# Kernel optimization log

Measured on AMD Instinct MI355X. Metric: run time of the kernel, lower is better.

## Reference

```python
import jax, jax.numpy as jnp
import numpy as np

H, W, A, C = 200, 704, 2, 256   # BEV grid, anchors, feature channels
NC, K = 4, 20000                # peer CAVs, selected anchors per CAV
REG = 7 * A                     # reg head channels


def setup_inputs() -> dict:
    key = jax.random.key(0)
    ks = jax.random.split(key, 8)
    feat = jax.random.normal(ks[0], (1, C, H, W), jnp.float32)
    cls_w = jax.random.normal(ks[1], (A, C), jnp.float32) * 0.02
    cls_b = jnp.zeros((A,), jnp.float32)
    reg_w = jax.random.normal(ks[2], (REG, C), jnp.float32) * 0.02
    reg_b = jnp.zeros((REG,), jnp.float32)
    psm_v2x = jax.random.normal(ks[3], (NC, K), jnp.float32)
    rm_v2x = jax.random.normal(ks[4], (NC, 7 * K), jnp.float32)
    scores_v2x = jax.random.uniform(ks[5], (NC, K), jnp.float32, 0.3, 1.0)
    flat = A * H * W
    idx = []
    for i in range(NC):  # unique sorted flat indices per CAV (masked_select semantics)
        perm = jax.random.permutation(jax.random.fold_in(ks[6], i), flat)[:K]
        idx.append(jnp.sort(perm))
    mask_idx = jnp.stack(idx).astype(jnp.int32)
    # mask_reg = mask.repeat(1,7,1,1): indices tile with offsets r*A*H*W
    offs = (jnp.arange(7) * flat).astype(jnp.int32)
    mask_reg_idx = (mask_idx[:, None, :] + offs[None, :, None]).reshape(NC, 7 * K)
    return {
        'spatial_features_2d': feat, 'cls_w': cls_w, 'cls_b': cls_b,
        'reg_w': reg_w, 'reg_b': reg_b, 'psm_v2x': psm_v2x, 'rm_v2x': rm_v2x,
        'scores_v2x': scores_v2x, 'mask_idx': mask_idx, 'mask_reg_idx': mask_reg_idx,
    }


def _restore(vals, idx, shape):
    # restore_tensor: scatter compacted values into zeros at flat indices, per CAV
    n = vals.shape[0]
    flat = int(np.prod(shape))
    out = jnp.zeros((n, flat), vals.dtype)
    out = out.at[jnp.arange(n)[:, None], idx].set(vals)
    return out.reshape((n,) + shape)


def reference(spatial_features_2d, cls_w, cls_b, reg_w, reg_b,
              psm_v2x, rm_v2x, scores_v2x, mask_idx, mask_reg_idx):
    # 1x1 conv heads
    psm_single = jnp.einsum('bchw,ac->bahw', spatial_features_2d, cls_w) + cls_b[None, :, None, None]
    rm_single = jnp.einsum('bchw,rc->brhw', spatial_features_2d, reg_w) + reg_b[None, :, None, None]
    prob = jax.nn.sigmoid(psm_single)
    # scatter-restore peer CAV results onto the BEV grid
    r_psm = _restore(psm_v2x, mask_idx, (A, H, W))        # [NC,A,H,W]
    r_scores = _restore(scores_v2x, mask_idx, (A, H, W))
    r_rm = _restore(rm_v2x, mask_reg_idx, (REG, H, W))    # [NC,14,H,W]
    psm_all = jnp.concatenate([psm_single, r_psm], axis=0)      # [1+NC,A,H,W]
    prob_all = jnp.concatenate([prob, r_scores], axis=0)
    rm_all = jnp.concatenate([rm_single, r_rm], axis=0)         # [1+NC,14,H,W]
    # per-cell winning CAV by score, then gather psm/rm from the winner
    cav = jnp.argmax(prob_all, axis=0)                    # [A,H,W]
    psm = jnp.take_along_axis(psm_all, cav[None], axis=0) # [1,A,H,W]
    cav_reg = jnp.tile(cav, (7, 1, 1))                    # [14,H,W]
    rm = jnp.take_along_axis(rm_all, cav_reg[None], axis=0)  # [1,14,H,W]
    return psm, rm
```

## Files before the change

### kernel.cpp

```cpp
#include <hip/hip_runtime.h>

#define HH 200
#define WW 704
#define HW (HH * WW)
#define HW2 (HW / 2)
#define AHW (2 * HW)
#define CC 256
#define NCAV 4
#define KK 20000
#define NJ 16
#define UPIPE 8

typedef unsigned int u32;

__global__ void scatter_best(const int* __restrict__ mask_idx,
                             const float* __restrict__ scores,
                             u32* __restrict__ winmap) {
    int t = blockIdx.x * blockDim.x + threadIdx.x;
    if (t >= NCAV * KK) return;
    int x = mask_idx[t];
    int n = t / KK;
    union { float f; u32 u; } s;
    s.f = scores[t];
    u32 pack = ((s.u - 0x3E800000u) << 7) | (u32)(3 - n);
    atomicMax(winmap + x, pack);
}

__device__ __forceinline__ int bsearch_row(const int* __restrict__ row, int x) {
    int lo = 0, hi = KK;
    while (lo < hi) {
        int mid = (lo + hi) >> 1;
        if (row[mid] < x) lo = mid + 1; else hi = mid;
    }
    return lo;
}

__global__ __launch_bounds__(64, 1) void head_select(
    const float2* __restrict__ feat2,
    const float* __restrict__ cls_w,
    const float* __restrict__ reg_w,
    const float* __restrict__ cls_b,
    const float* __restrict__ reg_b,
    const float* __restrict__ psm_v2x,
    const float* __restrict__ rm_v2x,
    const int* __restrict__ mask_idx,
    const u32* __restrict__ winmap,
    float* __restrict__ out) {
    __shared__ float w_lds[CC * NJ];

    int tid = threadIdx.x;
    for (int i = tid; i < CC * NJ; i += 64) {
        int j = i >> 8, c = i & 255;
        w_lds[c * NJ + j] = (j < 2) ? cls_w[j * CC + c] : reg_w[(j - 2) * CC + c];
    }
    __syncthreads();

    int q = blockIdx.x * 64 + tid;
    int pos = q * 2;

    float acc[2][NJ];
#pragma unroll
    for (int j = 0; j < NJ; ++j) {
        float b = (j < 2) ? cls_b[j] : reg_b[j - 2];
        acc[0][j] = b; acc[1][j] = b;
    }

    const float2* fp = feat2 + q;

    float2 A[UPIPE], B[UPIPE];
#pragma unroll
    for (int u = 0; u < UPIPE; ++u) A[u] = fp[u * HW2];

    for (int cb = 0; cb < CC; cb += 2 * UPIPE) {
#pragma unroll
        for (int u = 0; u < UPIPE; ++u) B[u] = fp[(cb + UPIPE + u) * HW2];
#pragma unroll
        for (int u = 0; u < UPIPE; ++u) {
            int c = cb + u;
            const float4* wv = (const float4*)&w_lds[c * NJ];
            float w[NJ];
            *(float4*)&w[0]  = wv[0];
            *(float4*)&w[4]  = wv[1];
            *(float4*)&w[8]  = wv[2];
            *(float4*)&w[12] = wv[3];
#pragma unroll
            for (int j = 0; j < NJ; ++j) {
                acc[0][j] += A[u].x * w[j];
                acc[1][j] += A[u].y * w[j];
            }
        }
#pragma unroll
        for (int u = 0; u < UPIPE; ++u) {
            int cn = cb + 2 * UPIPE + u;
            A[u] = fp[(cn < CC ? cn : 0) * HW2];
        }
#pragma unroll
        for (int u = 0; u < UPIPE; ++u) {
            int c = cb + UPIPE + u;
            const float4* wv = (const float4*)&w_lds[c * NJ];
            float w[NJ];
            *(float4*)&w[0]  = wv[0];
            *(float4*)&w[4]  = wv[1];
            *(float4*)&w[8]  = wv[2];
            *(float4*)&w[12] = wv[3];
#pragma unroll
            for (int j = 0; j < NJ; ++j) {
                acc[0][j] += B[u].x * w[j];
                acc[1][j] += B[u].y * w[j];
            }
        }
    }

    float2* out2 = (float2*)out;
#pragma unroll
    for (int a = 0; a < 2; ++a) {
        float ps[2], rm[7][2];
#pragma unroll
        for (int e = 0; e < 2; ++e) {
            float p = acc[e][a];
            float prob = 1.0f / (1.0f + expf(-p));
            int x = a * HW + pos + e;
            u32 win = winmap[x];
            float sc = 0.0f;
            if (win != 0u) {
                union { u32 u; float f; } v;
                v.u = (win >> 7) + 0x3E800000u;
                sc = v.f;
            }
            if (sc > prob) {
                int n = 3 - (int)(win & 3u);
                int k = bsearch_row(mask_idx + n * KK, x);
                ps[e] = psm_v2x[n * KK + k];
#pragma unroll
                for (int r = 0; r < 7; ++r)
                    rm[r][e] = rm_v2x[n * (7 * KK) + r * KK + k];
            } else {
                ps[e] = p;
#pragma unroll
                for (int r = 0; r < 7; ++r)
                    rm[r][e] = acc[e][2 + 2 * r + a];
            }
        }
        out2[a * HW2 + q] = make_float2(ps[0], ps[1]);
#pragma unroll
        for (int r = 0; r < 7; ++r)
            out2[HW + (2 * r + a) * HW2 + q] = make_float2(rm[r][0], rm[r][1]);
    }
}

extern "C" void kernel_launch(void* const* d_in, const int* in_sizes, int n_in,
                              void* d_out, int out_size, void* d_ws, size_t ws_size,
                              hipStream_t stream) {
    const float* feat    = (const float*)d_in[0];
    const float* cls_w   = (const float*)d_in[1];
    const float* cls_b   = (const float*)d_in[2];
    const float* reg_w   = (const float*)d_in[3];
    const float* reg_b   = (const float*)d_in[4];
    const float* psm_v2x = (const float*)d_in[5];
    const float* rm_v2x  = (const float*)d_in[6];
    const float* scores  = (const float*)d_in[7];
    const int* mask_idx  = (const int*)d_in[8];

    const size_t win_bytes = (size_t)AHW * sizeof(u32);
    u32* winmap = (ws_size >= win_bytes) ? (u32*)d_ws : (u32*)d_in[9];

    hipMemsetAsync(winmap, 0, win_bytes, stream);

    scatter_best<<<(NCAV * KK + 255) / 256, 256, 0, stream>>>(mask_idx, scores, winmap);
    head_select<<<HW2 / 64, 64, 0, stream>>>(
        (const float2*)feat, cls_w, reg_w, cls_b, reg_b,
        psm_v2x, rm_v2x, mask_idx, winmap, (float*)d_out);
}
```

Before: 249.4 us.

## Split channel reduction across four waves per block with LDS reduction

Each block now uses four wavefronts, and each wave accumulates a 64-channel slice of the 1x1 conv for the same 128 pixels. The partial sums go to LDS and are reduced by the first 128 threads, which then run the sigmoid, the winner selection and the output writes. This gives more waves per CU and more loads in flight to hide memory latency in a bandwidth-bound kernel. In exchange it adds two block barriers and an LDS reduction, leaves only half the threads active in the epilogue, and replaces float2 output stores with scalar stores.

```diff
diff --git a/kernel.cpp b/kernel.cpp
--- a/kernel.cpp
+++ b/kernel.cpp
@@ -10,6 +10,7 @@
 #define KK 20000
 #define NJ 16
 #define UPIPE 8
+#define CPW 64
 
 typedef unsigned int u32;
 
@@ -35,7 +36,7 @@
     return lo;
 }
 
-__global__ __launch_bounds__(64, 1) void head_select(
+__global__ __launch_bounds__(256, 4) void head_select(
     const float2* __restrict__ feat2,
     const float* __restrict__ cls_w,
     const float* __restrict__ reg_w,
@@ -46,80 +47,92 @@
     const int* __restrict__ mask_idx,
     const u32* __restrict__ winmap,
     float* __restrict__ out) {
-    __shared__ float w_lds[CC * NJ];
+    __shared__ float smem[8192];
 
     int tid = threadIdx.x;
-    for (int i = tid; i < CC * NJ; i += 64) {
+    int w = tid >> 6, lane = tid & 63;
+
+    for (int i = tid; i < CC * NJ; i += 256) {
         int j = i >> 8, c = i & 255;
-        w_lds[c * NJ + j] = (j < 2) ? cls_w[j * CC + c] : reg_w[(j - 2) * CC + c];
+        smem[c * NJ + j] = (j < 2) ? cls_w[j * CC + c] : reg_w[(j - 2) * CC + c];
     }
     __syncthreads();
 
-    int q = blockIdx.x * 64 + tid;
-    int pos = q * 2;
+    int q = blockIdx.x * 64 + lane;
+    const float2* fp = feat2 + q + (size_t)(w * CPW) * HW2;
 
     float acc[2][NJ];
 #pragma unroll
-    for (int j = 0; j < NJ; ++j) {
-        float b = (j < 2) ? cls_b[j] : reg_b[j - 2];
-        acc[0][j] = b; acc[1][j] = b;
-    }
-
-    const float2* fp = feat2 + q;
+    for (int j = 0; j < NJ; ++j) { acc[0][j] = 0.0f; acc[1][j] = 0.0f; }
 
     float2 A[UPIPE], B[UPIPE];
 #pragma unroll
     for (int u = 0; u < UPIPE; ++u) A[u] = fp[u * HW2];
 
-    for (int cb = 0; cb < CC; cb += 2 * UPIPE) {
+    for (int cb = 0; cb < CPW; cb += 2 * UPIPE) {
 #pragma unroll
         for (int u = 0; u < UPIPE; ++u) B[u] = fp[(cb + UPIPE + u) * HW2];
 #pragma unroll
         for (int u = 0; u < UPIPE; ++u) {
-            int c = cb + u;
-            const float4* wv = (const float4*)&w_lds[c * NJ];
-            float w[NJ];
-            *(float4*)&w[0]  = wv[0];
-            *(float4*)&w[4]  = wv[1];
-            *(float4*)&w[8]  = wv[2];
-            *(float4*)&w[12] = wv[3];
+            const float4* wv = (const float4*)&smem[(w * CPW + cb + u) * NJ];
+            float wt[NJ];
+            *(float4*)&wt[0]  = wv[0];
+            *(float4*)&wt[4]  = wv[1];
+            *(float4*)&wt[8]  = wv[2];
+            *(float4*)&wt[12] = wv[3];
 #pragma unroll
             for (int j = 0; j < NJ; ++j) {
-                acc[0][j] += A[u].x * w[j];
-                acc[1][j] += A[u].y * w[j];
+                acc[0][j] += A[u].x * wt[j];
+                acc[1][j] += A[u].y * wt[j];
             }
         }
 #pragma unroll
         for (int u = 0; u < UPIPE; ++u) {
             int cn = cb + 2 * UPIPE + u;
-            A[u] = fp[(cn < CC ? cn : 0) * HW2];
+            A[u] = fp[(cn < CPW ? cn : 0) * HW2];
         }
 #pragma unroll
         for (int u = 0; u < UPIPE; ++u) {
-            int c = cb + UPIPE + u;
-            const float4* wv = (const float4*)&w_lds[c * NJ];
-            float w[NJ];
-            *(float4*)&w[0]  = wv[0];
-            *(float4*)&w[4]  = wv[1];
-            *(float4*)&w[8]  = wv[2];
-            *(float4*)&w[12] = wv[3];
+            const float4* wv = (const float4*)&smem[(w * CPW + cb + UPIPE + u) * NJ];
+            float wt[NJ];
+            *(float4*)&wt[0]  = wv[0];
+            *(float4*)&wt[4]  = wv[1];
+            *(float4*)&wt[8]  = wv[2];
+            *(float4*)&wt[12] = wv[3];
 #pragma unroll
             for (int j = 0; j < NJ; ++j) {
-                acc[0][j] += B[u].x * w[j];
-                acc[1][j] += B[u].y * w[j];
+                acc[0][j] += B[u].x * wt[j];
+                acc[1][j] += B[u].y * wt[j];
             }
         }
     }
+    __syncthreads();
 
-    float2* out2 = (float2*)out;
 #pragma unroll
-    for (int a = 0; a < 2; ++a) {
-        float ps[2], rm[7][2];
+    for (int e = 0; e < 2; ++e)
 #pragma unroll
-        for (int e = 0; e < 2; ++e) {
-            float p = acc[e][a];
-            float prob = 1.0f / (1.0f + expf(-p));
-            int x = a * HW + pos + e;
+        for (int j = 0; j < NJ; ++j)
+            smem[(e * NJ + j) * 256 + tid] = acc[e][j];
+    __syncthreads();
+
+    if (tid < 128) {
+        int g = tid >> 1, e = tid & 1;
+        int p = blockIdx.x * 128 + tid;
+        float val[NJ];
+#pragma unroll
+        for (int j = 0; j < NJ; ++j) {
+            float b = (j < 2) ? cls_b[j] : reg_b[j - 2];
+            float s = b;
+#pragma unroll
+            for (int wv = 0; wv < 4; ++wv)
+                s += smem[(e * NJ + j) * 256 + wv * 64 + g];
+            val[j] = s;
+        }
+#pragma unroll
+        for (int a = 0; a < 2; ++a) {
+            float pv = val[a];
+            float prob = 1.0f / (1.0f + expf(-pv));
+            int x = a * HW + p;
             u32 win = winmap[x];
             float sc = 0.0f;
             if (win != 0u) {
@@ -130,21 +143,18 @@
             if (sc > prob) {
                 int n = 3 - (int)(win & 3u);
                 int k = bsearch_row(mask_idx + n * KK, x);
-                ps[e] = psm_v2x[n * KK + k];
+                out[x] = psm_v2x[n * KK + k];
 #pragma unroll
                 for (int r = 0; r < 7; ++r)
-                    rm[r][e] = rm_v2x[n * (7 * KK) + r * KK + k];
+                    out[AHW + (2 * r + a) * HW + p] =
+                        rm_v2x[n * (7 * KK) + r * KK + k];
             } else {
-                ps[e] = p;
+                out[x] = pv;
 #pragma unroll
                 for (int r = 0; r < 7; ++r)
-                    rm[r][e] = acc[e][2 + 2 * r + a];
+                    out[AHW + (2 * r + a) * HW + p] = val[2 + 2 * r + a];
             }
         }
-        out2[a * HW2 + q] = make_float2(ps[0], ps[1]);
-#pragma unroll
-        for (int r = 0; r < 7; ++r)
-            out2[HW + (2 * r + a) * HW2 + q] = make_float2(rm[r][0], rm[r][1]);
     }
 }
 
@@ -167,7 +177,7 @@
     hipMemsetAsync(winmap, 0, win_bytes, stream);
 
     scatter_best<<<(NCAV * KK + 255) / 256, 256, 0, stream>>>(mask_idx, scores, winmap);
-    head_select<<<HW2 / 64, 64, 0, stream>>>(
+    head_select<<<HW2 / 64, 256, 0, stream>>>(
         (const float2*)feat, cls_w, reg_w, cls_b, reg_b,
         psm_v2x, rm_v2x, mask_idx, winmap, (float*)d_out);
 }
```

New measurement: 250.2 us. No clear change (+0.4%).
